# Performance work log

Hardware: AMD Instinct MI355X
Metric: run time of the kernel (lower is better)

The kernel has to match this reference:

```python
import jax, jax.numpy as jnp
import numpy as np

N_NODES = 100000
N_EDGES = 1600000
D_FEAT = 128
UNITS = 128


def setup_inputs() -> dict:
    key = jax.random.key(0)
    k = jax.random.split(key, 7)
    x = jax.random.normal(k[0], (N_NODES, D_FEAT), dtype=jnp.float32)
    edge_row = jax.random.randint(k[1], (N_EDGES,), 0, N_NODES, dtype=jnp.int32)
    edge_col = jax.random.randint(k[2], (N_EDGES,), 0, N_NODES, dtype=jnp.int32)
    edge_vals = jax.random.uniform(k[3], (N_EDGES,), dtype=jnp.float32)
    W = jax.random.normal(k[4], (D_FEAT, UNITS), dtype=jnp.float32) * 0.05
    W_gate = jax.random.normal(k[5], (D_FEAT, 1), dtype=jnp.float32) * 0.05
    b_gate = jax.random.normal(k[6], (1,), dtype=jnp.float32) * 0.05
    return {"x": x, "edge_row": edge_row, "edge_col": edge_col,
            "edge_vals": edge_vals, "W": W, "W_gate": W_gate, "b_gate": b_gate}


def reference(x, edge_row, edge_col, edge_vals, W, W_gate, b_gate):
    # pre_sup = X @ W  -> [N, units]
    pre_sup = x @ W
    # gate g = sigmoid(X @ W_gate + b_gate)  -> [N, 1]
    g = jax.nn.sigmoid(x @ W_gate + b_gate)
    h = g * pre_sup  # [N, units]
    # output = A @ h, A in COO form (row, col, vals):
    # out[r] = sum_e vals[e] * h[col[e]] for edges with row[e] == r
    msgs = edge_vals[:, None] * h[edge_col]  # [E, units]
    out = jax.ops.segment_sum(msgs, edge_row, num_segments=N_NODES)
    # activation is None (linear)
    return out
```

## Files before the change

kernel.cpp:

```cpp
#include <hip/hip_runtime.h>
#include <hip/hip_bf16.h>

constexpr int D        = 128;
constexpr int BM       = 64;
constexpr int CHUNK    = 4096;
constexpr int NBKT_PAD = 1024;
constexpr int BKT_CAP  = 3072;
constexpr int BKT_STRIDE = 4096;
constexpr int OVF_CAP  = 65536;

typedef __attribute__((ext_vector_type(8))) short bf16x8;
typedef __attribute__((ext_vector_type(4))) float f32x4;

__device__ __forceinline__ unsigned short rne_bf16(float f) {
    unsigned u = __float_as_uint(f);
    return (unsigned short)((u + 0x7FFF + ((u >> 16) & 1)) >> 16);
}

__global__ __launch_bounds__(256) void transpose_W(
    const float* __restrict__ W, unsigned short* __restrict__ wt_sw)
{
    int idx = blockIdx.x * 256 + threadIdx.x;
    int k = idx >> 7, f = idx & 127;
    wt_sw[f * 128 + (k ^ ((f & 7) << 3))] = rne_bf16(W[idx]);
}

__global__ __launch_bounds__(256) void mfma_gemm_gate(
    const float* __restrict__ x, const unsigned short* __restrict__ wt_sw,
    const float* __restrict__ Wg, const float* __restrict__ bg,
    __hip_bfloat16* __restrict__ h, int n_nodes)
{
    __shared__ __align__(16) char smem[49664];
    unsigned short* Ahi = (unsigned short*)smem;
    unsigned short* Bt  = Ahi + 64 * 128;
    float*          Gs  = (float*)(Bt + 128 * 128);
    unsigned short* Cbuf = (unsigned short*)smem;

    const int t    = threadIdx.x;
    const int lane = t & 63;
    const int w    = t >> 6;
    const int node0 = blockIdx.x * BM;

    #pragma unroll
    for (int i = 0; i < 8; ++i) {
        int e0 = (i * 256 + t) * 8;
        *(int4*)&Bt[e0] = *(const int4*)&wt_sw[e0];
    }

    #pragma unroll
    for (int i = 0; i < 8; ++i) {
        int fidx = (i * 256 + t) * 4;
        int row  = fidx >> 7;
        int k    = fidx & 127;
        int node = node0 + row;
        float4 v = make_float4(0.f, 0.f, 0.f, 0.f);
        if (node < n_nodes) v = *(const float4*)(x + (size_t)node * D + k);
        unsigned long long pk =
            (unsigned long long)rne_bf16(v.x) |
            ((unsigned long long)rne_bf16(v.y) << 16) |
            ((unsigned long long)rne_bf16(v.z) << 32) |
            ((unsigned long long)rne_bf16(v.w) << 48);
        int eidx = row * 128 + (k ^ ((row & 7) << 3));
        *(unsigned long long*)&Ahi[eidx] = pk;
    }
    __syncthreads();

    if (t < BM) {
        float gp = 0.f;
        #pragma unroll
        for (int kq = 0; kq < 16; ++kq) {
            int eidx = t * 128 + ((kq * 8) ^ ((t & 7) << 3));
            unsigned long long a = *(const unsigned long long*)&Ahi[eidx];
            unsigned long long b = *(const unsigned long long*)&Ahi[eidx + 4];
            #pragma unroll
            for (int j = 0; j < 4; ++j) {
                gp += __uint_as_float((unsigned)((a >> (16 * j)) & 0xFFFF) << 16) * Wg[kq * 8 + j];
                gp += __uint_as_float((unsigned)((b >> (16 * j)) & 0xFFFF) << 16) * Wg[kq * 8 + 4 + j];
            }
        }
        Gs[t] = 1.f / (1.f + __expf(-(gp + bg[0])));
    }

    f32x4 acc[4][2];
    #pragma unroll
    for (int m = 0; m < 4; ++m)
        #pragma unroll
        for (int n = 0; n < 2; ++n)
            acc[m][n] = (f32x4){0.f, 0.f, 0.f, 0.f};

    #pragma unroll
    for (int kk = 0; kk < 4; ++kk) {
        const int k0 = kk * 32 + (lane >> 4) * 8;
        bf16x8 bfr[2];
        #pragma unroll
        for (int n = 0; n < 2; ++n) {
            int f = w * 32 + n * 16 + (lane & 15);
            bfr[n] = *(const bf16x8*)&Bt[f * 128 + (k0 ^ ((f & 7) << 3))];
        }
        #pragma unroll
        for (int m = 0; m < 4; ++m) {
            int row = m * 16 + (lane & 15);
            bf16x8 ah = *(const bf16x8*)&Ahi[row * 128 + (k0 ^ ((row & 7) << 3))];
            #pragma unroll
            for (int n = 0; n < 2; ++n)
                acc[m][n] = __builtin_amdgcn_mfma_f32_16x16x32_bf16(ah, bfr[n], acc[m][n], 0, 0, 0);
        }
    }
    __syncthreads();

    #pragma unroll
    for (int m = 0; m < 4; ++m) {
        #pragma unroll
        for (int n = 0; n < 2; ++n) {
            int feat = w * 32 + n * 16 + (lane & 15);
            #pragma unroll
            for (int j = 0; j < 4; ++j) {
                int rloc = m * 16 + (lane >> 4) * 4 + j;
                Cbuf[rloc * 136 + feat] = rne_bf16(acc[m][n][j] * Gs[rloc]);
            }
        }
    }
    __syncthreads();

    {
        int row  = t >> 2;
        int fb   = (t & 3) * 32;
        int node = node0 + row;
        if (node < n_nodes) {
            __hip_bfloat16* hp = h + (size_t)node * D + fb;
            #pragma unroll
            for (int q = 0; q < 4; ++q)
                *(int4*)(hp + q * 8) = *(const int4*)&Cbuf[row * 136 + fb + q * 8];
        }
    }
}

__global__ __launch_bounds__(256) void bin_pass(
    const int* __restrict__ er, const int* __restrict__ ec,
    const float* __restrict__ ev, int* __restrict__ gcursor,
    uint2* __restrict__ bucketArr, int* __restrict__ ovfCur,
    uint4* __restrict__ ovfArr, int n_edges)
{
    __shared__ uint2 staged[CHUNK];
    __shared__ unsigned short bkt_of[CHUNK];
    __shared__ int lcnt[NBKT_PAD];
    __shared__ int lbase[NBKT_PAD];
    __shared__ int gbase[NBKT_PAD];
    __shared__ int wt[4];

    const int t = threadIdx.x;
    const int lane = t & 63, w = t >> 6;
    const int e0 = blockIdx.x * CHUNK;
    const int ecnt = min(CHUNK, n_edges - e0);

    for (int i = t; i < NBKT_PAD; i += 256) lcnt[i] = 0;
    __syncthreads();

    for (int i = t; i < ecnt; i += 256) atomicAdd(&lcnt[er[e0 + i] >> 7], 1);
    __syncthreads();

    {
        const int base = t * 4;
        int v[4], tsum = 0;
        #pragma unroll
        for (int j = 0; j < 4; ++j) { v[j] = lcnt[base + j]; tsum += v[j]; }
        int x = tsum;
        #pragma unroll
        for (int d = 1; d < 64; d <<= 1) {
            int y = __shfl_up(x, d);
            if (lane >= d) x += y;
        }
        if (lane == 63) wt[w] = x;
        __syncthreads();
        int woff = 0;
        for (int i = 0; i < w; ++i) woff += wt[i];
        int run = woff + x - tsum;
        #pragma unroll
        for (int j = 0; j < 4; ++j) { lbase[base + j] = run; run += v[j]; lcnt[base + j] = 0; }
    }
    __syncthreads();

    for (int i = t; i < ecnt; i += 256) {
        int r = er[e0 + i];
        int b = r >> 7;
        int p = lbase[b] + atomicAdd(&lcnt[b], 1);
        staged[p] = make_uint2((unsigned)ec[e0 + i] | ((unsigned)(r & 127) << 17),
                               (unsigned)__float_as_int(ev[e0 + i]));
        bkt_of[p] = (unsigned short)b;
    }
    __syncthreads();

    for (int i = t; i < NBKT_PAD; i += 256) {
        int c = lcnt[i];
        if (c) gbase[i] = atomicAdd(&gcursor[i], c);
    }
    __syncthreads();

    for (int i = t; i < ecnt; i += 256) {
        int b = bkt_of[i];
        int pos = gbase[b] + (i - lbase[b]);
        uint2 pe = staged[i];
        if (pos < BKT_STRIDE) {
            bucketArr[(size_t)b * BKT_STRIDE + pos] = pe;
        } else {
            int op = atomicAdd(ovfCur, 1);
            if (op < OVF_CAP) ovfArr[op] = make_uint4((unsigned)b, pe.x, pe.y, 0u);
        }
    }
}

__global__ __launch_bounds__(256) void sort_gather(
    const int* __restrict__ gcursor, const uint2* __restrict__ bucketArr,
    const int* __restrict__ ovfCur, const uint4* __restrict__ ovfArr,
    const __hip_bfloat16* __restrict__ h, float* __restrict__ out, int n_nodes)
{
    __shared__ uint2 sEdges[BKT_CAP];
    __shared__ int rcnt[128];
    __shared__ int rbase[129];
    __shared__ int rfill[128];
    __shared__ int wt2[2];

    const int t = threadIdx.x, lane = t & 63, w = t >> 6;
    const int b = blockIdx.x;
    const int r0 = b << 7;
    const size_t s = (size_t)b * BKT_STRIDE;
    const int total = gcursor[b];
    const int cnt = min(total, BKT_STRIDE);
    const bool ovf = cnt > BKT_CAP;
    const int ovfN = (total > BKT_STRIDE || *ovfCur > 0) ? min(*ovfCur, OVF_CAP) : 0;

    if (t < 128) rcnt[t] = 0;
    __syncthreads();

    if (!ovf) {
        for (int i = t; i < cnt; i += 256)
            atomicAdd(&rcnt[(bucketArr[s + i].x >> 17) & 127], 1);
    }
    __syncthreads();

    {
        int v = 0, x = 0;
        if (t < 128) {
            v = rcnt[t];
            x = v;
            #pragma unroll
            for (int d = 1; d < 64; d <<= 1) {
                int y = __shfl_up(x, d);
                if (lane >= d) x += y;
            }
            if (lane == 63) wt2[w] = x;
        }
        __syncthreads();
        if (t < 128) {
            int rb = (w ? wt2[0] : 0) + x - v;
            rbase[t] = rb;
            rfill[t] = rb;
        }
        if (t == 0) rbase[128] = cnt;
    }
    __syncthreads();

    if (!ovf) {
        for (int i = t; i < cnt; i += 256) {
            uint2 pe = bucketArr[s + i];
            int rl = (pe.x >> 17) & 127;
            int p  = atomicAdd(&rfill[rl], 1);
            sEdges[p] = pe;
        }
    }
    __syncthreads();

    const int g = lane >> 4;
    const int p = lane & 15;

    for (int k = 0; k < 32; ++k) {
        const int rl = w + (k << 2);
        const int row = r0 + rl;
        if (row >= n_nodes) continue;

        float acc[8];
        #pragma unroll
        for (int j = 0; j < 8; ++j) acc[j] = 0.f;

        if (!ovf) {
            const int rs = rbase[rl], re = rbase[rl + 1];
            for (int bb = rs; bb < re; bb += 8) {
                int i0 = bb + g;
                int i1 = i0 + 4;
                float v0 = 0.f, v1 = 0.f;
                int c0 = 0, c1 = 0;
                if (i0 < re) { uint2 pk = sEdges[i0]; v0 = __uint_as_float(pk.y); c0 = (int)(pk.x & 0x1FFFFu); }
                if (i1 < re) { uint2 pk = sEdges[i1]; v1 = __uint_as_float(pk.y); c1 = (int)(pk.x & 0x1FFFFu); }
                const int4 h0 = *(const int4*)(h + (size_t)c0 * D + p * 8);
                const int4 h1 = *(const int4*)(h + (size_t)c1 * D + p * 8);
                {
                    unsigned d0 = (unsigned)h0.x, d1 = (unsigned)h0.y, d2 = (unsigned)h0.z, d3 = (unsigned)h0.w;
                    acc[0] += v0 * __uint_as_float(d0 << 16);
                    acc[1] += v0 * __uint_as_float(d0 & 0xFFFF0000u);
                    acc[2] += v0 * __uint_as_float(d1 << 16);
                    acc[3] += v0 * __uint_as_float(d1 & 0xFFFF0000u);
                    acc[4] += v0 * __uint_as_float(d2 << 16);
                    acc[5] += v0 * __uint_as_float(d2 & 0xFFFF0000u);
                    acc[6] += v0 * __uint_as_float(d3 << 16);
                    acc[7] += v0 * __uint_as_float(d3 & 0xFFFF0000u);
                }
                {
                    unsigned d0 = (unsigned)h1.x, d1 = (unsigned)h1.y, d2 = (unsigned)h1.z, d3 = (unsigned)h1.w;
                    acc[0] += v1 * __uint_as_float(d0 << 16);
                    acc[1] += v1 * __uint_as_float(d0 & 0xFFFF0000u);
                    acc[2] += v1 * __uint_as_float(d1 << 16);
                    acc[3] += v1 * __uint_as_float(d1 & 0xFFFF0000u);
                    acc[4] += v1 * __uint_as_float(d2 << 16);
                    acc[5] += v1 * __uint_as_float(d2 & 0xFFFF0000u);
                    acc[6] += v1 * __uint_as_float(d3 << 16);
                    acc[7] += v1 * __uint_as_float(d3 & 0xFFFF0000u);
                }
            }
        } else {
            const unsigned target = (unsigned)rl;
            for (int bb = 0; bb < cnt; bb += 8) {
                int i0 = bb + g;
                int i1 = i0 + 4;
                float v0 = 0.f, v1 = 0.f;
                int c0 = 0, c1 = 0;
                if (i0 < cnt) {
                    uint2 pk = bucketArr[s + i0];
                    if (((pk.x >> 17) & 127u) == target) { v0 = __uint_as_float(pk.y); c0 = (int)(pk.x & 0x1FFFFu); }
                }
                if (i1 < cnt) {
                    uint2 pk = bucketArr[s + i1];
                    if (((pk.x >> 17) & 127u) == target) { v1 = __uint_as_float(pk.y); c1 = (int)(pk.x & 0x1FFFFu); }
                }
                const int4 h0 = *(const int4*)(h + (size_t)c0 * D + p * 8);
                const int4 h1 = *(const int4*)(h + (size_t)c1 * D + p * 8);
                {
                    unsigned d0 = (unsigned)h0.x, d1 = (unsigned)h0.y, d2 = (unsigned)h0.z, d3 = (unsigned)h0.w;
                    acc[0] += v0 * __uint_as_float(d0 << 16);
                    acc[1] += v0 * __uint_as_float(d0 & 0xFFFF0000u);
                    acc[2] += v0 * __uint_as_float(d1 << 16);
                    acc[3] += v0 * __uint_as_float(d1 & 0xFFFF0000u);
                    acc[4] += v0 * __uint_as_float(d2 << 16);
                    acc[5] += v0 * __uint_as_float(d2 & 0xFFFF0000u);
                    acc[6] += v0 * __uint_as_float(d3 << 16);
                    acc[7] += v0 * __uint_as_float(d3 & 0xFFFF0000u);
                }
                {
                    unsigned d0 = (unsigned)h1.x, d1 = (unsigned)h1.y, d2 = (unsigned)h1.z, d3 = (unsigned)h1.w;
                    acc[0] += v1 * __uint_as_float(d0 << 16);
                    acc[1] += v1 * __uint_as_float(d0 & 0xFFFF0000u);
                    acc[2] += v1 * __uint_as_float(d1 << 16);
                    acc[3] += v1 * __uint_as_float(d1 & 0xFFFF0000u);
                    acc[4] += v1 * __uint_as_float(d2 << 16);
                    acc[5] += v1 * __uint_as_float(d2 & 0xFFFF0000u);
                    acc[6] += v1 * __uint_as_float(d3 << 16);
                    acc[7] += v1 * __uint_as_float(d3 & 0xFFFF0000u);
                }
            }
        }

        if (ovfN > 0 && g == 0) {
            for (int j = 0; j < ovfN; ++j) {
                uint4 oe = ovfArr[j];
                if (oe.x == (unsigned)b && ((oe.y >> 17) & 127u) == (unsigned)rl) {
                    float v = __uint_as_float(oe.z);
                    int col = (int)(oe.y & 0x1FFFFu);
                    const int4 hv = *(const int4*)(h + (size_t)col * D + p * 8);
                    unsigned d0 = (unsigned)hv.x, d1 = (unsigned)hv.y, d2 = (unsigned)hv.z, d3 = (unsigned)hv.w;
                    acc[0] += v * __uint_as_float(d0 << 16);
                    acc[1] += v * __uint_as_float(d0 & 0xFFFF0000u);
                    acc[2] += v * __uint_as_float(d1 << 16);
                    acc[3] += v * __uint_as_float(d1 & 0xFFFF0000u);
                    acc[4] += v * __uint_as_float(d2 << 16);
                    acc[5] += v * __uint_as_float(d2 & 0xFFFF0000u);
                    acc[6] += v * __uint_as_float(d3 << 16);
                    acc[7] += v * __uint_as_float(d3 & 0xFFFF0000u);
                }
            }
        }

        #pragma unroll
        for (int j = 0; j < 8; ++j) {
            acc[j] += __shfl_xor(acc[j], 16);
            acc[j] += __shfl_xor(acc[j], 32);
        }

        if (lane < 16) {
            float* op = out + (size_t)row * D + lane * 8;
            *(float4*)(op)     = make_float4(acc[0], acc[1], acc[2], acc[3]);
            *(float4*)(op + 4) = make_float4(acc[4], acc[5], acc[6], acc[7]);
        }
    }
}

__global__ __launch_bounds__(256) void scatter_edges(
    const int* __restrict__ er, const int* __restrict__ ec,
    const float* __restrict__ ev, const __hip_bfloat16* __restrict__ h,
    float* __restrict__ out, int n_edges)
{
    int gw   = (blockIdx.x * 256 + threadIdx.x) >> 6;
    int lane = threadIdx.x & 63;
    if (gw >= n_edges) return;
    int r = er[gw];
    int c = ec[gw];
    float v = ev[gw];
    unsigned hv = *(const unsigned*)(h + (size_t)c * D + lane * 2);
    float* op = out + (size_t)r * D + lane * 2;
    atomicAdd(op,     v * __uint_as_float(hv << 16));
    atomicAdd(op + 1, v * __uint_as_float(hv & 0xFFFF0000u));
}

extern "C" void kernel_launch(void* const* d_in, const int* in_sizes, int n_in,
                              void* d_out, int out_size, void* d_ws, size_t ws_size,
                              hipStream_t stream) {
    const float* x  = (const float*)d_in[0];
    const int*   er = (const int*)d_in[1];
    const int*   ec = (const int*)d_in[2];
    const float* ev = (const float*)d_in[3];
    const float* W  = (const float*)d_in[4];
    const float* Wg = (const float*)d_in[5];
    const float* bg = (const float*)d_in[6];
    float* out = (float*)d_out;

    const int n_nodes = in_sizes[0] / D;
    const int n_edges = in_sizes[1];
    const int nbkt = (n_nodes + 127) >> 7;

    char* ws = (char*)d_ws;
    size_t off = 0;
    auto alloc = [&](size_t bytes) {
        char* p = ws + off;
        off += (bytes + 15) & ~size_t(15);
        return p;
    };
    __hip_bfloat16* h = (__hip_bfloat16*)alloc((size_t)n_nodes * D * sizeof(__hip_bfloat16));
    unsigned short* wt_sw = (unsigned short*)alloc((size_t)D * D * sizeof(unsigned short));
    uint2* bucketArr = (uint2*)alloc((size_t)nbkt * BKT_STRIDE * sizeof(uint2));
    int*   gcursor   = (int*)  alloc(NBKT_PAD * sizeof(int));
    int*   ovfCur    = (int*)  alloc(16);
    uint4* ovfArr    = (uint4*)alloc((size_t)OVF_CAP * sizeof(uint4));
    bool have_ws = off <= ws_size;

    transpose_W<<<D * D / 256, 256, 0, stream>>>(W, wt_sw);

    dim3 gemm_grid((n_nodes + BM - 1) / BM);
    mfma_gemm_gate<<<gemm_grid, 256, 0, stream>>>(x, wt_sw, Wg, bg, h, n_nodes);

    if (have_ws) {
        hipMemsetAsync(gcursor, 0, NBKT_PAD * sizeof(int) + 16, stream);
        int cb = (n_edges + CHUNK - 1) / CHUNK;
        bin_pass<<<cb, 256, 0, stream>>>(er, ec, ev, gcursor, bucketArr, ovfCur, ovfArr, n_edges);
        sort_gather<<<nbkt, 256, 0, stream>>>(gcursor, bucketArr, ovfCur, ovfArr, h, out, n_nodes);
    } else {
        hipMemsetAsync(d_out, 0, (size_t)out_size * sizeof(float), stream);
        int blocks = (n_edges + 3) / 4;
        scatter_edges<<<blocks, 256, 0, stream>>>(er, ec, ev, h, out, n_edges);
    }
}
```

Before: 134.1 us.

## Split each sort_gather bucket across two blocks, halve bin_pass chunk size

```diff
diff --git a/kernel.cpp b/kernel.cpp
--- a/kernel.cpp
+++ b/kernel.cpp
@@ -3,9 +3,9 @@
 
 constexpr int D        = 128;
 constexpr int BM       = 64;
-constexpr int CHUNK    = 4096;
+constexpr int CHUNK    = 2048;
 constexpr int NBKT_PAD = 1024;
-constexpr int BKT_CAP  = 3072;
+constexpr int SUB_CAP  = 1536;
 constexpr int BKT_STRIDE = 4096;
 constexpr int OVF_CAP  = 65536;
 
@@ -214,58 +214,54 @@
     const int* __restrict__ ovfCur, const uint4* __restrict__ ovfArr,
     const __hip_bfloat16* __restrict__ h, float* __restrict__ out, int n_nodes)
 {
-    __shared__ uint2 sEdges[BKT_CAP];
-    __shared__ int rcnt[128];
-    __shared__ int rbase[129];
-    __shared__ int rfill[128];
-    __shared__ int wt2[2];
+    __shared__ uint2 sEdges[SUB_CAP];
+    __shared__ int rcnt[64];
+    __shared__ int rbase[65];
+    __shared__ int rfill[64];
 
     const int t = threadIdx.x, lane = t & 63, w = t >> 6;
-    const int b = blockIdx.x;
-    const int r0 = b << 7;
+    const int b    = blockIdx.x >> 1;
+    const int half = blockIdx.x & 1;
+    const int r0   = (b << 7) + (half << 6);
     const size_t s = (size_t)b * BKT_STRIDE;
     const int total = gcursor[b];
     const int cnt = min(total, BKT_STRIDE);
-    const bool ovf = cnt > BKT_CAP;
     const int ovfN = (total > BKT_STRIDE || *ovfCur > 0) ? min(*ovfCur, OVF_CAP) : 0;
 
-    if (t < 128) rcnt[t] = 0;
-    __syncthreads();
-
-    if (!ovf) {
-        for (int i = t; i < cnt; i += 256)
-            atomicAdd(&rcnt[(bucketArr[s + i].x >> 17) & 127], 1);
-    }
-    __syncthreads();
-
-    {
-        int v = 0, x = 0;
-        if (t < 128) {
-            v = rcnt[t];
-            x = v;
-            #pragma unroll
-            for (int d = 1; d < 64; d <<= 1) {
-                int y = __shfl_up(x, d);
-                if (lane >= d) x += y;
-            }
-            if (lane == 63) wt2[w] = x;
-        }
-        __syncthreads();
-        if (t < 128) {
-            int rb = (w ? wt2[0] : 0) + x - v;
-            rbase[t] = rb;
-            rfill[t] = rb;
-        }
-        if (t == 0) rbase[128] = cnt;
-    }
-    __syncthreads();
+    if (t < 64) rcnt[t] = 0;
+    __syncthreads();
+
+    for (int i = t; i < cnt; i += 256) {
+        int rl = (int)((bucketArr[s + i].x >> 17) & 127u);
+        if ((rl >> 6) == half) atomicAdd(&rcnt[rl & 63], 1);
+    }
+    __syncthreads();
+
+    if (t < 64) {
+        int v = rcnt[t];
+        int x = v;
+        #pragma unroll
+        for (int d = 1; d < 64; d <<= 1) {
+            int y = __shfl_up(x, d);
+            if (lane >= d) x += y;
+        }
+        rbase[t] = x - v;
+        rfill[t] = x - v;
+        if (t == 63) rbase[64] = x;
+    }
+    __syncthreads();
+
+    const int halfCnt = rbase[64];
+    const bool ovf = halfCnt > SUB_CAP;
 
     if (!ovf) {
         for (int i = t; i < cnt; i += 256) {
             uint2 pe = bucketArr[s + i];
-            int rl = (pe.x >> 17) & 127;
-            int p  = atomicAdd(&rfill[rl], 1);
-            sEdges[p] = pe;
+            int rl = (int)((pe.x >> 17) & 127u);
+            if ((rl >> 6) == half) {
+                int p = atomicAdd(&rfill[rl & 63], 1);
+                sEdges[p] = pe;
+            }
         }
     }
     __syncthreads();
@@ -273,7 +269,7 @@
     const int g = lane >> 4;
     const int p = lane & 15;
 
-    for (int k = 0; k < 32; ++k) {
+    for (int k = 0; k < 16; ++k) {
         const int rl = w + (k << 2);
         const int row = r0 + rl;
         if (row >= n_nodes) continue;
@@ -317,7 +313,7 @@
                 }
             }
         } else {
-            const unsigned target = (unsigned)rl;
+            const unsigned target = (unsigned)(half * 64 + rl);
             for (int bb = 0; bb < cnt; bb += 8) {
                 int i0 = bb + g;
                 int i1 = i0 + 4;
@@ -359,9 +355,10 @@
         }
 
         if (ovfN > 0 && g == 0) {
+            const unsigned target = (unsigned)(half * 64 + rl);
             for (int j = 0; j < ovfN; ++j) {
                 uint4 oe = ovfArr[j];
-                if (oe.x == (unsigned)b && ((oe.y >> 17) & 127u) == (unsigned)rl) {
+                if (oe.x == (unsigned)b && ((oe.y >> 17) & 127u) == target) {
                     float v = __uint_as_float(oe.z);
                     int col = (int)(oe.y & 0x1FFFFu);
                     const int4 hv = *(const int4*)(h + (size_t)col * D + p * 8);
@@ -449,7 +446,7 @@
         hipMemsetAsync(gcursor, 0, NBKT_PAD * sizeof(int) + 16, stream);
         int cb = (n_edges + CHUNK - 1) / CHUNK;
         bin_pass<<<cb, 256, 0, stream>>>(er, ec, ev, gcursor, bucketArr, ovfCur, ovfArr, n_edges);
-        sort_gather<<<nbkt, 256, 0, stream>>>(gcursor, bucketArr, ovfCur, ovfArr, h, out, n_nodes);
+        sort_gather<<<nbkt * 2, 256, 0, stream>>>(gcursor, bucketArr, ovfCur, ovfArr, h, out, n_nodes);
     } else {
         hipMemsetAsync(d_out, 0, (size_t)out_size * sizeof(float), stream);
         int blocks = (n_edges + 3) / 4;
```

New measurement: 145.0 us. 1.08x slower.

## Merge GEMM+gate and edge binning into one heterogeneous-block kernel

Applied to the files above, without the earlier changes.

```diff
diff --git a/kernel.cpp b/kernel.cpp
--- a/kernel.cpp
+++ b/kernel.cpp
@@ -8,6 +8,7 @@
 constexpr int BKT_CAP  = 3072;
 constexpr int BKT_STRIDE = 4096;
 constexpr int OVF_CAP  = 65536;
+constexpr int EPT      = CHUNK / 256;
 
 typedef __attribute__((ext_vector_type(8))) short bf16x8;
 typedef __attribute__((ext_vector_type(4))) float f32x4;
@@ -25,186 +26,199 @@
     wt_sw[f * 128 + (k ^ ((f & 7) << 3))] = rne_bf16(W[idx]);
 }
 
-__global__ __launch_bounds__(256) void mfma_gemm_gate(
+__global__ __launch_bounds__(256) void gemm_bin(
     const float* __restrict__ x, const unsigned short* __restrict__ wt_sw,
     const float* __restrict__ Wg, const float* __restrict__ bg,
-    __hip_bfloat16* __restrict__ h, int n_nodes)
+    __hip_bfloat16* __restrict__ h,
+    const int* __restrict__ er, const int* __restrict__ ec,
+    const float* __restrict__ ev, int* __restrict__ gcursor,
+    uint2* __restrict__ bucketArr, int* __restrict__ ovfCur,
+    uint4* __restrict__ ovfArr,
+    int n_nodes, int n_edges, int gemm_blocks)
 {
-    __shared__ __align__(16) char smem[49664];
-    unsigned short* Ahi = (unsigned short*)smem;
-    unsigned short* Bt  = Ahi + 64 * 128;
-    float*          Gs  = (float*)(Bt + 128 * 128);
-    unsigned short* Cbuf = (unsigned short*)smem;
+    __shared__ __align__(16) char smem[53264];
 
     const int t    = threadIdx.x;
     const int lane = t & 63;
     const int w    = t >> 6;
-    const int node0 = blockIdx.x * BM;
-
-    #pragma unroll
-    for (int i = 0; i < 8; ++i) {
-        int e0 = (i * 256 + t) * 8;
-        *(int4*)&Bt[e0] = *(const int4*)&wt_sw[e0];
-    }
-
-    #pragma unroll
-    for (int i = 0; i < 8; ++i) {
-        int fidx = (i * 256 + t) * 4;
-        int row  = fidx >> 7;
-        int k    = fidx & 127;
-        int node = node0 + row;
-        float4 v = make_float4(0.f, 0.f, 0.f, 0.f);
-        if (node < n_nodes) v = *(const float4*)(x + (size_t)node * D + k);
-        unsigned long long pk =
-            (unsigned long long)rne_bf16(v.x) |
-            ((unsigned long long)rne_bf16(v.y) << 16) |
-            ((unsigned long long)rne_bf16(v.z) << 32) |
-            ((unsigned long long)rne_bf16(v.w) << 48);
-        int eidx = row * 128 + (k ^ ((row & 7) << 3));
-        *(unsigned long long*)&Ahi[eidx] = pk;
-    }
-    __syncthreads();
-
-    if (t < BM) {
-        float gp = 0.f;
-        #pragma unroll
-        for (int kq = 0; kq < 16; ++kq) {
-            int eidx = t * 128 + ((kq * 8) ^ ((t & 7) << 3));
-            unsigned long long a = *(const unsigned long long*)&Ahi[eidx];
-            unsigned long long b = *(const unsigned long long*)&Ahi[eidx + 4];
-            #pragma unroll
-            for (int j = 0; j < 4; ++j) {
-                gp += __uint_as_float((unsigned)((a >> (16 * j)) & 0xFFFF) << 16) * Wg[kq * 8 + j];
-                gp += __uint_as_float((unsigned)((b >> (16 * j)) & 0xFFFF) << 16) * Wg[kq * 8 + 4 + j];
-            }
-        }
-        Gs[t] = 1.f / (1.f + __expf(-(gp + bg[0])));
-    }
-
-    f32x4 acc[4][2];
-    #pragma unroll
-    for (int m = 0; m < 4; ++m)
-        #pragma unroll
-        for (int n = 0; n < 2; ++n)
-            acc[m][n] = (f32x4){0.f, 0.f, 0.f, 0.f};
-
-    #pragma unroll
-    for (int kk = 0; kk < 4; ++kk) {
-        const int k0 = kk * 32 + (lane >> 4) * 8;
-        bf16x8 bfr[2];
-        #pragma unroll
-        for (int n = 0; n < 2; ++n) {
-            int f = w * 32 + n * 16 + (lane & 15);
-            bfr[n] = *(const bf16x8*)&Bt[f * 128 + (k0 ^ ((f & 7) << 3))];
-        }
+
+    if ((int)blockIdx.x < gemm_blocks) {
+        unsigned short* Ahi = (unsigned short*)smem;
+        unsigned short* Bt  = Ahi + 64 * 128;
+        float*          Gs  = (float*)(Bt + 128 * 128);
+        unsigned short* Cbuf = (unsigned short*)smem;
+
+        const int node0 = blockIdx.x * BM;
+
+        #pragma unroll
+        for (int i = 0; i < 8; ++i) {
+            int e0 = (i * 256 + t) * 8;
+            *(int4*)&Bt[e0] = *(const int4*)&wt_sw[e0];
+        }
+
+        #pragma unroll
+        for (int i = 0; i < 8; ++i) {
+            int fidx = (i * 256 + t) * 4;
+            int row  = fidx >> 7;
+            int k    = fidx & 127;
+            int node = node0 + row;
+            float4 v = make_float4(0.f, 0.f, 0.f, 0.f);
+            if (node < n_nodes) v = *(const float4*)(x + (size_t)node * D + k);
+            unsigned long long pk =
+                (unsigned long long)rne_bf16(v.x) |
+                ((unsigned long long)rne_bf16(v.y) << 16) |
+                ((unsigned long long)rne_bf16(v.z) << 32) |
+                ((unsigned long long)rne_bf16(v.w) << 48);
+            int eidx = row * 128 + (k ^ ((row & 7) << 3));
+            *(unsigned long long*)&Ahi[eidx] = pk;
+        }
+        __syncthreads();
+
+        if (t < BM) {
+            float gp = 0.f;
+            #pragma unroll
+            for (int kq = 0; kq < 16; ++kq) {
+                int eidx = t * 128 + ((kq * 8) ^ ((t & 7) << 3));
+                unsigned long long a = *(const unsigned long long*)&Ahi[eidx];
+                unsigned long long b = *(const unsigned long long*)&Ahi[eidx + 4];
+                #pragma unroll
+                for (int j = 0; j < 4; ++j) {
+                    gp += __uint_as_float((unsigned)((a >> (16 * j)) & 0xFFFF) << 16) * Wg[kq * 8 + j];
+                    gp += __uint_as_float((unsigned)((b >> (16 * j)) & 0xFFFF) << 16) * Wg[kq * 8 + 4 + j];
+                }
+            }
+            Gs[t] = 1.f / (1.f + __expf(-(gp + bg[0])));
+        }
+
+        f32x4 acc[4][2];
+        #pragma unroll
+        for (int m = 0; m < 4; ++m)
+            #pragma unroll
+            for (int n = 0; n < 2; ++n)
+                acc[m][n] = (f32x4){0.f, 0.f, 0.f, 0.f};
+
+        #pragma unroll
+        for (int kk = 0; kk < 4; ++kk) {
+            const int k0 = kk * 32 + (lane >> 4) * 8;
+            bf16x8 bfr[2];
+            #pragma unroll
+            for (int n = 0; n < 2; ++n) {
+                int f = w * 32 + n * 16 + (lane & 15);
+                bfr[n] = *(const bf16x8*)&Bt[f * 128 + (k0 ^ ((f & 7) << 3))];
+            }
+            #pragma unroll
+            for (int m = 0; m < 4; ++m) {
+                int row = m * 16 + (lane & 15);
+                bf16x8 ah = *(const bf16x8*)&Ahi[row * 128 + (k0 ^ ((row & 7) << 3))];
+                #pragma unroll
+                for (int n = 0; n < 2; ++n)
+                    acc[m][n] = __builtin_amdgcn_mfma_f32_16x16x32_bf16(ah, bfr[n], acc[m][n], 0, 0, 0);
+            }
+        }
+        __syncthreads();
+
         #pragma unroll
         for (int m = 0; m < 4; ++m) {
-            int row = m * 16 + (lane & 15);
-            bf16x8 ah = *(const bf16x8*)&Ahi[row * 128 + (k0 ^ ((row & 7) << 3))];
-            #pragma unroll
-            for (int n = 0; n < 2; ++n)
-                acc[m][n] = __builtin_amdgcn_mfma_f32_16x16x32_bf16(ah, bfr[n], acc[m][n], 0, 0, 0);
-        }
-    }
-    __syncthreads();
-
-    #pragma unroll
-    for (int m = 0; m < 4; ++m) {
-        #pragma unroll
-        for (int n = 0; n < 2; ++n) {
-            int feat = w * 32 + n * 16 + (lane & 15);
-            #pragma unroll
-            for (int j = 0; j < 4; ++j) {
-                int rloc = m * 16 + (lane >> 4) * 4 + j;
-                Cbuf[rloc * 136 + feat] = rne_bf16(acc[m][n][j] * Gs[rloc]);
-            }
-        }
-    }
-    __syncthreads();
-
-    {
-        int row  = t >> 2;
-        int fb   = (t & 3) * 32;
-        int node = node0 + row;
-        if (node < n_nodes) {
-            __hip_bfloat16* hp = h + (size_t)node * D + fb;
-            #pragma unroll
-            for (int q = 0; q < 4; ++q)
-                *(int4*)(hp + q * 8) = *(const int4*)&Cbuf[row * 136 + fb + q * 8];
-        }
-    }
-}
-
-__global__ __launch_bounds__(256) void bin_pass(
-    const int* __restrict__ er, const int* __restrict__ ec,
-    const float* __restrict__ ev, int* __restrict__ gcursor,
-    uint2* __restrict__ bucketArr, int* __restrict__ ovfCur,
-    uint4* __restrict__ ovfArr, int n_edges)
-{
-    __shared__ uint2 staged[CHUNK];
-    __shared__ unsigned short bkt_of[CHUNK];
-    __shared__ int lcnt[NBKT_PAD];
-    __shared__ int lbase[NBKT_PAD];
-    __shared__ int gbase[NBKT_PAD];
-    __shared__ int wt[4];
-
-    const int t = threadIdx.x;
-    const int lane = t & 63, w = t >> 6;
-    const int e0 = blockIdx.x * CHUNK;
-    const int ecnt = min(CHUNK, n_edges - e0);
-
-    for (int i = t; i < NBKT_PAD; i += 256) lcnt[i] = 0;
-    __syncthreads();
-
-    for (int i = t; i < ecnt; i += 256) atomicAdd(&lcnt[er[e0 + i] >> 7], 1);
-    __syncthreads();
-
-    {
-        const int base = t * 4;
-        int v[4], tsum = 0;
-        #pragma unroll
-        for (int j = 0; j < 4; ++j) { v[j] = lcnt[base + j]; tsum += v[j]; }
-        int x = tsum;
-        #pragma unroll
-        for (int d = 1; d < 64; d <<= 1) {
-            int y = __shfl_up(x, d);
-            if (lane >= d) x += y;
-        }
-        if (lane == 63) wt[w] = x;
-        __syncthreads();
-        int woff = 0;
-        for (int i = 0; i < w; ++i) woff += wt[i];
-        int run = woff + x - tsum;
-        #pragma unroll
-        for (int j = 0; j < 4; ++j) { lbase[base + j] = run; run += v[j]; lcnt[base + j] = 0; }
-    }
-    __syncthreads();
-
-    for (int i = t; i < ecnt; i += 256) {
-        int r = er[e0 + i];
-        int b = r >> 7;
-        int p = lbase[b] + atomicAdd(&lcnt[b], 1);
-        staged[p] = make_uint2((unsigned)ec[e0 + i] | ((unsigned)(r & 127) << 17),
-                               (unsigned)__float_as_int(ev[e0 + i]));
-        bkt_of[p] = (unsigned short)b;
-    }
-    __syncthreads();
-
-    for (int i = t; i < NBKT_PAD; i += 256) {
-        int c = lcnt[i];
-        if (c) gbase[i] = atomicAdd(&gcursor[i], c);
-    }
-    __syncthreads();
-
-    for (int i = t; i < ecnt; i += 256) {
-        int b = bkt_of[i];
-        int pos = gbase[b] + (i - lbase[b]);
-        uint2 pe = staged[i];
-        if (pos < BKT_STRIDE) {
-            bucketArr[(size_t)b * BKT_STRIDE + pos] = pe;
-        } else {
-            int op = atomicAdd(ovfCur, 1);
-            if (op < OVF_CAP) ovfArr[op] = make_uint4((unsigned)b, pe.x, pe.y, 0u);
+            #pragma unroll
+            for (int n = 0; n < 2; ++n) {
+                int feat = w * 32 + n * 16 + (lane & 15);
+                #pragma unroll
+                for (int j = 0; j < 4; ++j) {
+                    int rloc = m * 16 + (lane >> 4) * 4 + j;
+                    Cbuf[rloc * 136 + feat] = rne_bf16(acc[m][n][j] * Gs[rloc]);
+                }
+            }
+        }
+        __syncthreads();
+
+        {
+            int row  = t >> 2;
+            int fb   = (t & 3) * 32;
+            int node = node0 + row;
+            if (node < n_nodes) {
+                __hip_bfloat16* hp = h + (size_t)node * D + fb;
+                #pragma unroll
+                for (int q = 0; q < 4; ++q)
+                    *(int4*)(hp + q * 8) = *(const int4*)&Cbuf[row * 136 + fb + q * 8];
+            }
+        }
+    } else {
+        uint2* staged           = (uint2*)smem;
+        unsigned short* bkt_of  = (unsigned short*)(smem + 32768);
+        int* lcnt               = (int*)(smem + 40960);
+        int* lbase              = lcnt + NBKT_PAD;
+        int* gbase              = lbase + NBKT_PAD;
+        int* wt                 = gbase + NBKT_PAD;
+
+        const int bb = (int)blockIdx.x - gemm_blocks;
+        const int e0 = bb * CHUNK;
+        const int ecnt = min(CHUNK, n_edges - e0);
+
+        for (int i = t; i < NBKT_PAD; i += 256) lcnt[i] = 0;
+        __syncthreads();
+
+        int rcache[EPT];
+        #pragma unroll
+        for (int j = 0; j < EPT; ++j) {
+            int i = t + j * 256;
+            if (i < ecnt) {
+                rcache[j] = er[e0 + i];
+                atomicAdd(&lcnt[rcache[j] >> 7], 1);
+            } else rcache[j] = -1;
+        }
+        __syncthreads();
+
+        {
+            const int base = t * 4;
+            int v[4], tsum = 0;
+            #pragma unroll
+            for (int j = 0; j < 4; ++j) { v[j] = lcnt[base + j]; tsum += v[j]; }
+            int x2 = tsum;
+            #pragma unroll
+            for (int d = 1; d < 64; d <<= 1) {
+                int y = __shfl_up(x2, d);
+                if (lane >= d) x2 += y;
+            }
+            if (lane == 63) wt[w] = x2;
+            __syncthreads();
+            int woff = 0;
+            for (int i = 0; i < w; ++i) woff += wt[i];
+            int run = woff + x2 - tsum;
+            #pragma unroll
+            for (int j = 0; j < 4; ++j) { lbase[base + j] = run; run += v[j]; lcnt[base + j] = 0; }
+        }
+        __syncthreads();
+
+        #pragma unroll
+        for (int j = 0; j < EPT; ++j) {
+            int i = t + j * 256;
+            if (rcache[j] >= 0) {
+                int r = rcache[j];
+                int b = r >> 7;
+                int p = lbase[b] + atomicAdd(&lcnt[b], 1);
+                staged[p] = make_uint2((unsigned)ec[e0 + i] | ((unsigned)(r & 127) << 17),
+                                       (unsigned)__float_as_int(ev[e0 + i]));
+                bkt_of[p] = (unsigned short)b;
+            }
+        }
+        __syncthreads();
+
+        for (int i = t; i < NBKT_PAD; i += 256) {
+            int c = lcnt[i];
+            if (c) gbase[i] = atomicAdd(&gcursor[i], c);
+        }
+        __syncthreads();
+
+        for (int i = t; i < ecnt; i += 256) {
+            int b = bkt_of[i];
+            int pos = gbase[b] + (i - lbase[b]);
+            uint2 pe = staged[i];
+            if (pos < BKT_STRIDE) {
+                bucketArr[(size_t)b * BKT_STRIDE + pos] = pe;
+            } else {
+                int op = atomicAdd(ovfCur, 1);
+                if (op < OVF_CAP) ovfArr[op] = make_uint4((unsigned)b, pe.x, pe.y, 0u);
+            }
         }
     }
 }
@@ -409,6 +423,13 @@
     atomicAdd(op + 1, v * __uint_as_float(hv & 0xFFFF0000u));
 }
 
+__global__ __launch_bounds__(256) void mfma_gemm_only(
+    const float* __restrict__ x, const unsigned short* __restrict__ wt_sw,
+    const float* __restrict__ Wg, const float* __restrict__ bg,
+    __hip_bfloat16* __restrict__ h, int n_nodes)
+{
+}
+
 extern "C" void kernel_launch(void* const* d_in, const int* in_sizes, int n_in,
                               void* d_out, int out_size, void* d_ws, size_t ws_size,
                               hipStream_t stream) {
@@ -424,6 +445,8 @@
     const int n_nodes = in_sizes[0] / D;
     const int n_edges = in_sizes[1];
     const int nbkt = (n_nodes + 127) >> 7;
+    const int gemm_blocks = (n_nodes + BM - 1) / BM;
+    const int bin_blocks  = (n_edges + CHUNK - 1) / CHUNK;
 
     char* ws = (char*)d_ws;
     size_t off = 0;
@@ -442,15 +465,16 @@
 
     transpose_W<<<D * D / 256, 256, 0, stream>>>(W, wt_sw);
 
-    dim3 gemm_grid((n_nodes + BM - 1) / BM);
-    mfma_gemm_gate<<<gemm_grid, 256, 0, stream>>>(x, wt_sw, Wg, bg, h, n_nodes);
-
     if (have_ws) {
         hipMemsetAsync(gcursor, 0, NBKT_PAD * sizeof(int) + 16, stream);
-        int cb = (n_edges + CHUNK - 1) / CHUNK;
-        bin_pass<<<cb, 256, 0, stream>>>(er, ec, ev, gcursor, bucketArr, ovfCur, ovfArr, n_edges);
+        gemm_bin<<<gemm_blocks + bin_blocks, 256, 0, stream>>>(
+            x, wt_sw, Wg, bg, h, er, ec, ev, gcursor, bucketArr, ovfCur, ovfArr,
+            n_nodes, n_edges, gemm_blocks);
         sort_gather<<<nbkt, 256, 0, stream>>>(gcursor, bucketArr, ovfCur, ovfArr, h, out, n_nodes);
     } else {
+        gemm_bin<<<gemm_blocks, 256, 0, stream>>>(
+            x, wt_sw, Wg, bg, h, er, ec, ev, (int*)nullptr, (uint2*)nullptr,
+            (int*)nullptr, (uint4*)nullptr, n_nodes, n_edges, gemm_blocks);
         hipMemsetAsync(d_out, 0, (size_t)out_size * sizeof(float), stream);
         int blocks = (n_edges + 3) / 4;
         scatter_edges<<<blocks, 256, 0, stream>>>(er, ec, ev, h, out, n_edges);
```

Measured after the change: 126.3 us. 5.8% less time.
